# Kernel tuning notes

Hardware: AMD Instinct MI355X
Metric: run time of the kernel (lower is better)

The kernel has to match this reference:

```python
import jax, jax.numpy as jnp
import numpy as np

DIM = 1024
B, S = 4, 4096

def setup_inputs() -> dict:
    key = jax.random.key(0)
    ks = jax.random.split(key, 8)
    scale = 1.0 / np.sqrt(DIM)
    x = jax.random.normal(ks[0], (B, S, DIM), dtype=jnp.float32)
    Wk = jax.random.normal(ks[1], (DIM, DIM), dtype=jnp.float32) * scale
    Wv = jax.random.normal(ks[2], (DIM, DIM), dtype=jnp.float32) * scale
    Wr = jax.random.normal(ks[3], (DIM, DIM), dtype=jnp.float32) * scale
    Wo = jax.random.normal(ks[4], (DIM, DIM), dtype=jnp.float32) * scale
    time_decay = jax.random.normal(ks[5], (DIM,), dtype=jnp.float32) * 0.01 - 5.0
    time_first = jax.random.normal(ks[6], (DIM,), dtype=jnp.float32) * 0.01
    return {"x": x, "Wk": Wk, "Wv": Wv, "Wr": Wr, "Wo": Wo,
            "time_decay": time_decay, "time_first": time_first}

def reference(x, Wk, Wv, Wr, Wo, time_decay, time_first):
    # Projections (Linear with weight [out, in]: y = x @ W^T)
    k = jnp.einsum('bsd,ed->bse', x, Wk)
    v = jnp.einsum('bsd,ed->bse', x, Wv)
    r = jax.nn.sigmoid(jnp.einsum('bsd,ed->bse', x, Wr))
    w = -jnp.exp(time_decay)          # (D,)
    decay = jnp.exp(w)                # exp(w), per-channel decay in (0,1)
    eu = jnp.exp(time_first)          # exp(u)
    kv = k * v                        # (B, S, D)

    def step(state, kv_t):
        wkv = state + eu * kv_t       # output numerator this step
        new_state = decay * state + kv_t
        return new_state, wkv

    state0 = jnp.zeros((x.shape[0], x.shape[2]), dtype=x.dtype)
    # scan over time axis: move S to leading dim
    _, wkv_seq = jax.lax.scan(step, state0, jnp.swapaxes(kv, 0, 1))  # (S, B, D)
    out = r * jnp.swapaxes(wkv_seq, 0, 1)  # (B, S, D)
    return jnp.einsum('bsd,ed->bse', out, Wo)
```

## Files before the change

### kernel.cpp

```cpp
#include <hip/hip_runtime.h>
#include <hip/hip_bf16.h>

#define DIMD   1024
#define BATCH  4
#define SEQ    4096
#define NTOK   (BATCH * SEQ)
#define CHUNK  64
#define NCHUNK (SEQ / CHUNK)

#define BM 128
#define BN 128
#define BK 32

typedef unsigned short ushort_t;
typedef __attribute__((ext_vector_type(8))) __bf16   bf16x8;
typedef __attribute__((ext_vector_type(4))) float    f32x4;
typedef __attribute__((ext_vector_type(8))) ushort_t u16x8;

__device__ __forceinline__ float b2f(ushort_t u) {
    union { unsigned int i; float f; } x;
    x.i = ((unsigned int)u) << 16;
    return x.f;
}

__device__ __forceinline__ ushort_t f2b(float f) {
    union { float f; unsigned int i; } x;
    x.f = f;
    unsigned int r = x.i + 0x7fffu + ((x.i >> 16) & 1u);
    return (ushort_t)(r >> 16);
}

__global__ __launch_bounds__(256)
void conv_f2b(const float* __restrict__ src, ushort_t* __restrict__ dst, int n8)
{
    const int i = blockIdx.x * 256 + threadIdx.x;
    if (i >= n8) return;
    const float4* s4 = (const float4*)src;
    const float4 a = s4[i * 2];
    const float4 b = s4[i * 2 + 1];
    u16x8 o;
    o[0] = f2b(a.x); o[1] = f2b(a.y); o[2] = f2b(a.z); o[3] = f2b(a.w);
    o[4] = f2b(b.x); o[5] = f2b(b.y); o[6] = f2b(b.z); o[7] = f2b(b.w);
    *(u16x8*)(dst + (size_t)i * 8) = o;
}

__global__ __launch_bounds__(256)
void conv_w(const float* __restrict__ W0, const float* __restrict__ W1,
            const float* __restrict__ W2, const float* __restrict__ W3,
            ushort_t* __restrict__ dst)
{
    const int m = blockIdx.y;
    const float* src = (m == 0) ? W0 : (m == 1) ? W1 : (m == 2) ? W2 : W3;
    const int i = blockIdx.x * 256 + threadIdx.x;
    const float4* s4 = (const float4*)src;
    const float4 a = s4[i * 2];
    const float4 b = s4[i * 2 + 1];
    u16x8 o;
    o[0] = f2b(a.x); o[1] = f2b(a.y); o[2] = f2b(a.z); o[3] = f2b(a.w);
    o[4] = f2b(b.x); o[5] = f2b(b.y); o[6] = f2b(b.z); o[7] = f2b(b.w);
    *(u16x8*)(dst + (size_t)m * DIMD * DIMD + (size_t)i * 8) = o;
}

__global__ __launch_bounds__(256, 2)
void gemm_kvr(const ushort_t* __restrict__ A,
              const ushort_t* __restrict__ Wk,
              const ushort_t* __restrict__ Wv,
              const ushort_t* __restrict__ Wr,
              ushort_t* __restrict__ Okv,
              ushort_t* __restrict__ Or)
{
    __shared__ __align__(16) ushort_t As[BM * BK];
    __shared__ __align__(16) ushort_t Bk[BN * BK];
    __shared__ __align__(16) ushort_t Bv[BN * BK];
    __shared__ __align__(16) ushort_t Br[BN * BK];

    const int tid  = threadIdx.x;
    const int lane = tid & 63;
    const int wv   = tid >> 6;
    const int wr   = wv >> 1;
    const int wc   = wv & 1;
    const int lrow = lane & 15;
    const int kq   = lane >> 4;

    const int row0 = blockIdx.x * BM;
    const int e0   = blockIdx.y * BN;

    f32x4 ak[4][4], av[4][4], ar[4][4];
#pragma unroll
    for (int i = 0; i < 4; i++)
#pragma unroll
        for (int j = 0; j < 4; j++) {
            ak[i][j] = f32x4{0.f, 0.f, 0.f, 0.f};
            av[i][j] = f32x4{0.f, 0.f, 0.f, 0.f};
            ar[i][j] = f32x4{0.f, 0.f, 0.f, 0.f};
        }

    for (int kt = 0; kt < DIMD / BK; ++kt) {
        const int k0 = kt * BK;

        __syncthreads();

#pragma unroll
        for (int it = 0; it < 2; ++it) {
            const int chunk = tid + it * 256;
            const int r = chunk >> 2;
            const int c = (chunk & 3) << 3;
            const ushort_t* ga = A  + (size_t)(row0 + r) * DIMD + k0 + c;
            const ushort_t* gk = Wk + (size_t)(e0 + r) * DIMD + k0 + c;
            const ushort_t* gv = Wv + (size_t)(e0 + r) * DIMD + k0 + c;
            const ushort_t* gr = Wr + (size_t)(e0 + r) * DIMD + k0 + c;
            __builtin_amdgcn_global_load_lds(
                (__attribute__((address_space(1))) void*)ga,
                (__attribute__((address_space(3))) void*)((char*)As + chunk * 16),
                16, 0, 0);
            __builtin_amdgcn_global_load_lds(
                (__attribute__((address_space(1))) void*)gk,
                (__attribute__((address_space(3))) void*)((char*)Bk + chunk * 16),
                16, 0, 0);
            __builtin_amdgcn_global_load_lds(
                (__attribute__((address_space(1))) void*)gv,
                (__attribute__((address_space(3))) void*)((char*)Bv + chunk * 16),
                16, 0, 0);
            __builtin_amdgcn_global_load_lds(
                (__attribute__((address_space(1))) void*)gr,
                (__attribute__((address_space(3))) void*)((char*)Br + chunk * 16),
                16, 0, 0);
        }

        __syncthreads();

        bf16x8 af[4], bk4[4], bv4[4], br4[4];
#pragma unroll
        for (int i = 0; i < 4; i++)
            af[i] = *(const bf16x8*)(As + (wr * 64 + i * 16 + lrow) * BK + kq * 8);
#pragma unroll
        for (int j = 0; j < 4; j++) {
            bk4[j] = *(const bf16x8*)(Bk + (wc * 64 + j * 16 + lrow) * BK + kq * 8);
            bv4[j] = *(const bf16x8*)(Bv + (wc * 64 + j * 16 + lrow) * BK + kq * 8);
            br4[j] = *(const bf16x8*)(Br + (wc * 64 + j * 16 + lrow) * BK + kq * 8);
        }

#pragma unroll
        for (int i = 0; i < 4; i++)
#pragma unroll
            for (int j = 0; j < 4; j++) {
                ak[i][j] = __builtin_amdgcn_mfma_f32_16x16x32_bf16(
                    af[i], bk4[j], ak[i][j], 0, 0, 0);
                av[i][j] = __builtin_amdgcn_mfma_f32_16x16x32_bf16(
                    af[i], bv4[j], av[i][j], 0, 0, 0);
                ar[i][j] = __builtin_amdgcn_mfma_f32_16x16x32_bf16(
                    af[i], br4[j], ar[i][j], 0, 0, 0);
            }
    }

#pragma unroll
    for (int i = 0; i < 4; i++)
#pragma unroll
        for (int j = 0; j < 4; j++)
#pragma unroll
            for (int r = 0; r < 4; r++) {
                const int row = row0 + wr * 64 + i * 16 + kq * 4 + r;
                const int col = e0 + wc * 64 + j * 16 + lrow;
                const size_t o = (size_t)row * DIMD + col;
                Okv[o] = f2b(ak[i][j][r] * av[i][j][r]);
                Or[o]  = f2b(1.f / (1.f + __expf(-ar[i][j][r])));
            }
}

__global__ __launch_bounds__(256, 2)
void gemm_bt(const ushort_t* __restrict__ A,
             const ushort_t* __restrict__ W,
             float* __restrict__ Of)
{
    __shared__ __align__(16) ushort_t As[BM * BK];
    __shared__ __align__(16) ushort_t Bs[BN * BK];

    const int tid  = threadIdx.x;
    const int lane = tid & 63;
    const int wv   = tid >> 6;
    const int wr   = wv >> 1;
    const int wc   = wv & 1;
    const int lrow = lane & 15;
    const int kq   = lane >> 4;

    const int row0 = blockIdx.x * BM;
    const int e0   = blockIdx.y * BN;

    f32x4 acc[4][4];
#pragma unroll
    for (int i = 0; i < 4; i++)
#pragma unroll
        for (int j = 0; j < 4; j++)
            acc[i][j] = f32x4{0.f, 0.f, 0.f, 0.f};

    for (int kt = 0; kt < DIMD / BK; ++kt) {
        const int k0 = kt * BK;

        __syncthreads();

#pragma unroll
        for (int it = 0; it < 2; ++it) {
            const int chunk = tid + it * 256;
            const int r = chunk >> 2;
            const int c = (chunk & 3) << 3;
            const ushort_t* ga = A + (size_t)(row0 + r) * DIMD + k0 + c;
            const ushort_t* gb = W + (size_t)(e0 + r) * DIMD + k0 + c;
            __builtin_amdgcn_global_load_lds(
                (__attribute__((address_space(1))) void*)ga,
                (__attribute__((address_space(3))) void*)((char*)As + chunk * 16),
                16, 0, 0);
            __builtin_amdgcn_global_load_lds(
                (__attribute__((address_space(1))) void*)gb,
                (__attribute__((address_space(3))) void*)((char*)Bs + chunk * 16),
                16, 0, 0);
        }

        __syncthreads();

        bf16x8 af[4], bfr[4];
#pragma unroll
        for (int i = 0; i < 4; i++)
            af[i] = *(const bf16x8*)(As + (wr * 64 + i * 16 + lrow) * BK + kq * 8);
#pragma unroll
        for (int j = 0; j < 4; j++)
            bfr[j] = *(const bf16x8*)(Bs + (wc * 64 + j * 16 + lrow) * BK + kq * 8);

#pragma unroll
        for (int i = 0; i < 4; i++)
#pragma unroll
            for (int j = 0; j < 4; j++)
                acc[i][j] = __builtin_amdgcn_mfma_f32_16x16x32_bf16(
                    af[i], bfr[j], acc[i][j], 0, 0, 0);
    }

#pragma unroll
    for (int i = 0; i < 4; i++)
#pragma unroll
        for (int j = 0; j < 4; j++)
#pragma unroll
            for (int r = 0; r < 4; r++) {
                const int row = row0 + wr * 64 + i * 16 + kq * 4 + r;
                const int col = e0 + wc * 64 + j * 16 + lrow;
                Of[(size_t)row * DIMD + col] = acc[i][j][r];
            }
}

__global__ __launch_bounds__(256)
void chunk_agg(const ushort_t* __restrict__ kvb,
               const float* __restrict__ td, float* __restrict__ cs)
{
    const int t  = blockIdx.x * 256 + threadIdx.x;
    const int d0 = (t & (DIMD / 8 - 1)) * 8;
    const int bc = t >> 7;
    const int c  = bc & (NCHUNK - 1);
    const int b  = bc >> 6;

    float decay[8], s[8];
#pragma unroll
    for (int j = 0; j < 8; j++) {
        decay[j] = __expf(-__expf(td[d0 + j]));
        s[j] = 0.f;
    }

    size_t off = ((size_t)b * SEQ + (size_t)c * CHUNK) * DIMD + d0;
#pragma unroll 8
    for (int i = 0; i < CHUNK; i++) {
        const u16x8 kv8 = *(const u16x8*)(kvb + off);
#pragma unroll
        for (int j = 0; j < 8; j++)
            s[j] = decay[j] * s[j] + b2f(kv8[j]);
        off += DIMD;
    }

    float* dst = cs + ((size_t)bc * DIMD + d0);
    *(float4*)(dst)     = float4{s[0], s[1], s[2], s[3]};
    *(float4*)(dst + 4) = float4{s[4], s[5], s[6], s[7]};
}

__global__ __launch_bounds__(256)
void chunk_scan(float* __restrict__ cs, const float* __restrict__ td)
{
    const int idx = blockIdx.x * 256 + threadIdx.x;
    const int d = idx & (DIMD - 1);
    const int b = idx >> 10;

    const float w      = -__expf(td[d]);
    const float decayL = __expf(w * (float)CHUNK);

    float v[NCHUNK];
    const size_t base = ((size_t)b * NCHUNK) * DIMD + d;
#pragma unroll
    for (int c = 0; c < NCHUNK; c++)
        v[c] = cs[base + (size_t)c * DIMD];

    float st = 0.f;
#pragma unroll
    for (int c = 0; c < NCHUNK; c++) {
        const float sc = v[c];
        v[c] = st;
        st = decayL * st + sc;
    }

#pragma unroll
    for (int c = 0; c < NCHUNK; c++)
        cs[base + (size_t)c * DIMD] = v[c];
}

__global__ __launch_bounds__(256)
void emit(const ushort_t* __restrict__ kvb, const ushort_t* __restrict__ rb,
          const float* __restrict__ td, const float* __restrict__ tf,
          const float* __restrict__ cs, ushort_t* __restrict__ op)
{
    const int t  = blockIdx.x * 256 + threadIdx.x;
    const int d0 = (t & (DIMD / 8 - 1)) * 8;
    const int bc = t >> 7;
    const int c  = bc & (NCHUNK - 1);
    const int b  = bc >> 6;

    float decay[8], eu[8], st[8];
#pragma unroll
    for (int j = 0; j < 8; j++) {
        decay[j] = __expf(-__expf(td[d0 + j]));
        eu[j]    = __expf(tf[d0 + j]);
    }
    const float* csp = cs + ((size_t)bc * DIMD + d0);
    const float4 s0 = *(const float4*)csp;
    const float4 s1 = *(const float4*)(csp + 4);
    st[0] = s0.x; st[1] = s0.y; st[2] = s0.z; st[3] = s0.w;
    st[4] = s1.x; st[5] = s1.y; st[6] = s1.z; st[7] = s1.w;

    size_t off = ((size_t)b * SEQ + (size_t)c * CHUNK) * DIMD + d0;
#pragma unroll 8
    for (int i = 0; i < CHUNK; i++) {
        const u16x8 kv8 = *(const u16x8*)(kvb + off);
        const u16x8 r8  = *(const u16x8*)(rb + off);
        u16x8 o8;
#pragma unroll
        for (int j = 0; j < 8; j++) {
            const float kv = b2f(kv8[j]);
            o8[j] = f2b(b2f(r8[j]) * (st[j] + eu[j] * kv));
            st[j] = decay[j] * st[j] + kv;
        }
        *(u16x8*)(op + off) = o8;
        off += DIMD;
    }
}

extern "C" void kernel_launch(void* const* d_in, const int* in_sizes, int n_in,
                              void* d_out, int out_size, void* d_ws, size_t ws_size,
                              hipStream_t stream)
{
    const float* x  = (const float*)d_in[0];
    const float* Wk = (const float*)d_in[1];
    const float* Wv = (const float*)d_in[2];
    const float* Wr = (const float*)d_in[3];
    const float* Wo = (const float*)d_in[4];
    const float* td = (const float*)d_in[5];
    const float* tf = (const float*)d_in[6];

    ushort_t* xb  = (ushort_t*)d_ws;
    ushort_t* Wb  = xb + (size_t)NTOK * DIMD;
    ushort_t* Wkb = Wb;
    ushort_t* Wvb = Wb + (size_t)DIMD * DIMD;
    ushort_t* Wrb = Wb + 2 * (size_t)DIMD * DIMD;
    ushort_t* Wob = Wb + 3 * (size_t)DIMD * DIMD;
    float*    cs  = (float*)(Wb + 4 * (size_t)DIMD * DIMD);
    ushort_t* pbuf = xb;

    ushort_t* kvb = (ushort_t*)d_out;
    ushort_t* rb  = kvb + (size_t)NTOK * DIMD;
    float*    out = (float*)d_out;

    conv_f2b<<<NTOK * DIMD / 8 / 256, 256, 0, stream>>>(x, xb, NTOK * DIMD / 8);
    conv_w<<<dim3(DIMD * DIMD / 8 / 256, 4), 256, 0, stream>>>(Wk, Wv, Wr, Wo, Wb);

    gemm_kvr<<<dim3(NTOK / BM, DIMD / BN), 256, 0, stream>>>(
        xb, Wkb, Wvb, Wrb, kvb, rb);

    chunk_agg<<<BATCH * NCHUNK * (DIMD / 8) / 256, 256, 0, stream>>>(kvb, td, cs);

    chunk_scan<<<BATCH * DIMD / 256, 256, 0, stream>>>(cs, td);

    emit<<<BATCH * NCHUNK * (DIMD / 8) / 256, 256, 0, stream>>>(
        kvb, rb, td, tf, cs, pbuf);

    gemm_bt<<<dim3(NTOK / BM, DIMD / BN), 256, 0, stream>>>(pbuf, Wob, out);
}
```

Before: 338.9 us.

## Fuse chunk aggregation into KVR GEMM epilogue and narrow output tile to 64

Removes the separate chunk_agg pass, which re-read the whole bf16 kv tensor. The projection GEMM epilogue now computes each 64-row chunk's decayed sum of k*v directly from fp32 accumulators, using per-row exp weights and cross-lane shuffles. To keep register pressure manageable with three accumulators, the N tile shrinks from 128 to 64. That doubles the grid and re-reads the A tile more often. The chunk sum now uses unrounded fp32 kv, which differs slightly from the bf16-rounded values used later.

```diff
diff --git a/kernel.cpp b/kernel.cpp
--- a/kernel.cpp
+++ b/kernel.cpp
@@ -11,6 +11,7 @@
 #define BM 128
 #define BN 128
 #define BK 32
+#define BNF 64
 
 typedef unsigned short ushort_t;
 typedef __attribute__((ext_vector_type(8))) __bf16   bf16x8;
@@ -66,13 +67,15 @@
               const ushort_t* __restrict__ Wk,
               const ushort_t* __restrict__ Wv,
               const ushort_t* __restrict__ Wr,
+              const float* __restrict__ td,
               ushort_t* __restrict__ Okv,
-              ushort_t* __restrict__ Or)
+              ushort_t* __restrict__ Or,
+              float* __restrict__ cs)
 {
     __shared__ __align__(16) ushort_t As[BM * BK];
-    __shared__ __align__(16) ushort_t Bk[BN * BK];
-    __shared__ __align__(16) ushort_t Bv[BN * BK];
-    __shared__ __align__(16) ushort_t Br[BN * BK];
+    __shared__ __align__(16) ushort_t Bk[BNF * BK];
+    __shared__ __align__(16) ushort_t Bv[BNF * BK];
+    __shared__ __align__(16) ushort_t Br[BNF * BK];
 
     const int tid  = threadIdx.x;
     const int lane = tid & 63;
@@ -83,13 +86,13 @@
     const int kq   = lane >> 4;
 
     const int row0 = blockIdx.x * BM;
-    const int e0   = blockIdx.y * BN;
-
-    f32x4 ak[4][4], av[4][4], ar[4][4];
+    const int e0   = blockIdx.y * BNF;
+
+    f32x4 ak[4][2], av[4][2], ar[4][2];
 #pragma unroll
     for (int i = 0; i < 4; i++)
 #pragma unroll
-        for (int j = 0; j < 4; j++) {
+        for (int j = 0; j < 2; j++) {
             ak[i][j] = f32x4{0.f, 0.f, 0.f, 0.f};
             av[i][j] = f32x4{0.f, 0.f, 0.f, 0.f};
             ar[i][j] = f32x4{0.f, 0.f, 0.f, 0.f};
@@ -105,45 +108,48 @@
             const int chunk = tid + it * 256;
             const int r = chunk >> 2;
             const int c = (chunk & 3) << 3;
-            const ushort_t* ga = A  + (size_t)(row0 + r) * DIMD + k0 + c;
-            const ushort_t* gk = Wk + (size_t)(e0 + r) * DIMD + k0 + c;
-            const ushort_t* gv = Wv + (size_t)(e0 + r) * DIMD + k0 + c;
-            const ushort_t* gr = Wr + (size_t)(e0 + r) * DIMD + k0 + c;
+            const ushort_t* ga = A + (size_t)(row0 + r) * DIMD + k0 + c;
             __builtin_amdgcn_global_load_lds(
                 (__attribute__((address_space(1))) void*)ga,
                 (__attribute__((address_space(3))) void*)((char*)As + chunk * 16),
                 16, 0, 0);
-            __builtin_amdgcn_global_load_lds(
-                (__attribute__((address_space(1))) void*)gk,
-                (__attribute__((address_space(3))) void*)((char*)Bk + chunk * 16),
-                16, 0, 0);
-            __builtin_amdgcn_global_load_lds(
-                (__attribute__((address_space(1))) void*)gv,
-                (__attribute__((address_space(3))) void*)((char*)Bv + chunk * 16),
-                16, 0, 0);
-            __builtin_amdgcn_global_load_lds(
-                (__attribute__((address_space(1))) void*)gr,
-                (__attribute__((address_space(3))) void*)((char*)Br + chunk * 16),
+        }
+        {
+            const int r = tid >> 2;
+            const int c = (tid & 3) << 3;
+            const size_t go = (size_t)(e0 + r) * DIMD + k0 + c;
+            __builtin_amdgcn_global_load_lds(
+                (__attribute__((address_space(1))) void*)(Wk + go),
+                (__attribute__((address_space(3))) void*)((char*)Bk + tid * 16),
+                16, 0, 0);
+            __builtin_amdgcn_global_load_lds(
+                (__attribute__((address_space(1))) void*)(Wv + go),
+                (__attribute__((address_space(3))) void*)((char*)Bv + tid * 16),
+                16, 0, 0);
+            __builtin_amdgcn_global_load_lds(
+                (__attribute__((address_space(1))) void*)(Wr + go),
+                (__attribute__((address_space(3))) void*)((char*)Br + tid * 16),
                 16, 0, 0);
         }
 
         __syncthreads();
 
-        bf16x8 af[4], bk4[4], bv4[4], br4[4];
+        bf16x8 af[4], bk4[2], bv4[2], br4[2];
 #pragma unroll
         for (int i = 0; i < 4; i++)
             af[i] = *(const bf16x8*)(As + (wr * 64 + i * 16 + lrow) * BK + kq * 8);
 #pragma unroll
-        for (int j = 0; j < 4; j++) {
-            bk4[j] = *(const bf16x8*)(Bk + (wc * 64 + j * 16 + lrow) * BK + kq * 8);
-            bv4[j] = *(const bf16x8*)(Bv + (wc * 64 + j * 16 + lrow) * BK + kq * 8);
-            br4[j] = *(const bf16x8*)(Br + (wc * 64 + j * 16 + lrow) * BK + kq * 8);
-        }
-
-#pragma unroll
-        for (int i = 0; i < 4; i++)
-#pragma unroll
-            for (int j = 0; j < 4; j++) {
+        for (int j = 0; j < 2; j++) {
+            const int bo = (wc * 32 + j * 16 + lrow) * BK + kq * 8;
+            bk4[j] = *(const bf16x8*)(Bk + bo);
+            bv4[j] = *(const bf16x8*)(Bv + bo);
+            br4[j] = *(const bf16x8*)(Br + bo);
+        }
+
+#pragma unroll
+        for (int i = 0; i < 4; i++)
+#pragma unroll
+            for (int j = 0; j < 2; j++) {
                 ak[i][j] = __builtin_amdgcn_mfma_f32_16x16x32_bf16(
                     af[i], bk4[j], ak[i][j], 0, 0, 0);
                 av[i][j] = __builtin_amdgcn_mfma_f32_16x16x32_bf16(
@@ -156,15 +162,35 @@
 #pragma unroll
     for (int i = 0; i < 4; i++)
 #pragma unroll
-        for (int j = 0; j < 4; j++)
+        for (int j = 0; j < 2; j++)
 #pragma unroll
             for (int r = 0; r < 4; r++) {
                 const int row = row0 + wr * 64 + i * 16 + kq * 4 + r;
-                const int col = e0 + wc * 64 + j * 16 + lrow;
+                const int col = e0 + wc * 32 + j * 16 + lrow;
                 const size_t o = (size_t)row * DIMD + col;
                 Okv[o] = f2b(ak[i][j][r] * av[i][j][r]);
                 Or[o]  = f2b(1.f / (1.f + __expf(-ar[i][j][r])));
             }
+
+#pragma unroll
+    for (int j = 0; j < 2; j++) {
+        const int col = e0 + wc * 32 + j * 16 + lrow;
+        const float w = -__expf(td[col]);
+        float s = 0.f;
+#pragma unroll
+        for (int i = 0; i < 4; i++)
+#pragma unroll
+            for (int r = 0; r < 4; r++) {
+                const int rl = i * 16 + kq * 4 + r;
+                s += __expf(w * (float)(63 - rl)) * ak[i][j][r] * av[i][j][r];
+            }
+        s += __shfl_xor(s, 16);
+        s += __shfl_xor(s, 32);
+        if (kq == 0) {
+            const int gchunk = (row0 >> 6) + wr;
+            cs[(size_t)gchunk * DIMD + col] = s;
+        }
+    }
 }
 
 __global__ __launch_bounds__(256, 2)
@@ -243,38 +269,6 @@
                 const int col = e0 + wc * 64 + j * 16 + lrow;
                 Of[(size_t)row * DIMD + col] = acc[i][j][r];
             }
-}
-
-__global__ __launch_bounds__(256)
-void chunk_agg(const ushort_t* __restrict__ kvb,
-               const float* __restrict__ td, float* __restrict__ cs)
-{
-    const int t  = blockIdx.x * 256 + threadIdx.x;
-    const int d0 = (t & (DIMD / 8 - 1)) * 8;
-    const int bc = t >> 7;
-    const int c  = bc & (NCHUNK - 1);
-    const int b  = bc >> 6;
-
-    float decay[8], s[8];
-#pragma unroll
-    for (int j = 0; j < 8; j++) {
-        decay[j] = __expf(-__expf(td[d0 + j]));
-        s[j] = 0.f;
-    }
-
-    size_t off = ((size_t)b * SEQ + (size_t)c * CHUNK) * DIMD + d0;
-#pragma unroll 8
-    for (int i = 0; i < CHUNK; i++) {
-        const u16x8 kv8 = *(const u16x8*)(kvb + off);
-#pragma unroll
-        for (int j = 0; j < 8; j++)
-            s[j] = decay[j] * s[j] + b2f(kv8[j]);
-        off += DIMD;
-    }
-
-    float* dst = cs + ((size_t)bc * DIMD + d0);
-    *(float4*)(dst)     = float4{s[0], s[1], s[2], s[3]};
-    *(float4*)(dst + 4) = float4{s[4], s[5], s[6], s[7]};
 }
 
 __global__ __launch_bounds__(256)
@@ -374,10 +368,8 @@
     conv_f2b<<<NTOK * DIMD / 8 / 256, 256, 0, stream>>>(x, xb, NTOK * DIMD / 8);
     conv_w<<<dim3(DIMD * DIMD / 8 / 256, 4), 256, 0, stream>>>(Wk, Wv, Wr, Wo, Wb);
 
-    gemm_kvr<<<dim3(NTOK / BM, DIMD / BN), 256, 0, stream>>>(
-        xb, Wkb, Wvb, Wrb, kvb, rb);
-
-    chunk_agg<<<BATCH * NCHUNK * (DIMD / 8) / 256, 256, 0, stream>>>(kvb, td, cs);
+    gemm_kvr<<<dim3(NTOK / BM, DIMD / BNF), 256, 0, stream>>>(
+        xb, Wkb, Wvb, Wrb, td, kvb, rb, cs);
 
     chunk_scan<<<BATCH * DIMD / 256, 256, 0, stream>>>(cs, td);
 
```

Result: faster. 319.9 us (-5.6%).
